# Optimization experiments

Measured on AMD Instinct MI355X. Metric: run time of the kernel, lower is better.

## Reference

```python
import jax, jax.numpy as jnp
import numpy as np

B, F = 512, 512
K, D = 32, 16  # num_kernels, dim_per_kernel


def setup_inputs() -> dict:
    key = jax.random.key(0)
    kx, kt = jax.random.split(key)
    x = jax.random.normal(kx, (B, F), dtype=jnp.float32)
    # keras 'uniform' init is small-range uniform; scale similarly
    T = jax.random.uniform(kt, (F, K * D), dtype=jnp.float32, minval=-0.05, maxval=0.05)
    return {"x": x, "T": T}


def reference(x, T):
    # m: [B, K, D]
    m = (x @ T).reshape(-1, K, D)
    # all-pairs L1 distance per kernel: [B, B, K]
    abs_diffs = jnp.sum(jnp.abs(m[:, None, :, :] - m[None, :, :, :]), axis=-1)
    # minibatch features: sum_j exp(-||m_i - m_j||_1) -> [B, K]
    feats = jnp.sum(jnp.exp(-abs_diffs), axis=1)
    return jnp.concatenate([x, feats], axis=1)
```

## Files before the change

kernel.cpp:

```cpp
#include <hip/hip_runtime.h>
#include <hip/hip_bf16.h>
#include <math.h>

#define BSZ 512
#define FDIM 512
#define NK 32
#define DD 16
#define NDIM (NK*DD)
#define OUTW (FDIM + NK)

typedef __attribute__((ext_vector_type(8))) short short8;
typedef __attribute__((ext_vector_type(4))) float float4v;

static __device__ __forceinline__ short f2bf(float f) {
  return (short)__builtin_bit_cast(unsigned short, __float2bfloat16(f));
}

__global__ __launch_bounds__(256, 4) void k_gemm(
    const float* __restrict__ x, const float* __restrict__ T,
    float* __restrict__ m, float* __restrict__ out) {
  const int t  = threadIdx.x;
  const int b  = blockIdx.x;
  const int rg = b >> 5, cg = b & 31;
  const int r0 = rg * 16, c0 = cg * 16;
  const int lane = t & 63;
  const int w    = __builtin_amdgcn_readfirstlane(t >> 6);
  const int mi   = lane & 15;
  const int q    = lane >> 4;

  const int slice = b >> 3;
  const float4 w0 = ((const float4*)x)[(size_t)slice * 512 + t];
  const float4 w1 = ((const float4*)x)[(size_t)slice * 512 + t + 256];
  const float4 w2 = ((const float4*)T)[(size_t)slice * 512 + t];
  const float4 w3 = ((const float4*)T)[(size_t)slice * 512 + t + 256];
  const float sink = w0.x + w1.y + w2.z + w3.w;

  const float* __restrict__ xa = x + (size_t)(r0 + mi) * FDIM + 128 * w + 8 * q;
  const float* __restrict__ tb = T + (size_t)(128 * w + 8 * q) * NDIM + c0 + mi;
  float4 A[8];
  float  Bv[32];
#pragma unroll
  for (int j = 0; j < 4; ++j) {
    A[2 * j]     = *(const float4*)(xa + 32 * j);
    A[2 * j + 1] = *(const float4*)(xa + 32 * j + 4);
  }
#pragma unroll
  for (int j = 0; j < 4; ++j)
#pragma unroll
    for (int i = 0; i < 8; ++i)
      Bv[8 * j + i] = tb[(size_t)(32 * j + i) * NDIM];

  float4v acc = {0.f, 0.f, 0.f, 0.f};
#pragma unroll
  for (int j = 0; j < 4; ++j) {
    short8 af, bf;
    af[0] = f2bf(A[2*j].x);   af[1] = f2bf(A[2*j].y);
    af[2] = f2bf(A[2*j].z);   af[3] = f2bf(A[2*j].w);
    af[4] = f2bf(A[2*j+1].x); af[5] = f2bf(A[2*j+1].y);
    af[6] = f2bf(A[2*j+1].z); af[7] = f2bf(A[2*j+1].w);
#pragma unroll
    for (int i = 0; i < 8; ++i) bf[i] = f2bf(Bv[8 * j + i]);
    acc = __builtin_amdgcn_mfma_f32_16x16x32_bf16(af, bf, acc, 0, 0, 0);
  }

  __shared__ float red[4][16][16];
#pragma unroll
  for (int r = 0; r < 4; ++r) red[w][q * 4 + r][mi] = acc[r];
  __syncthreads();
  {
    const int orow = t >> 4, ocol = t & 15;
    const float s = red[0][orow][ocol] + red[1][orow][ocol] +
                    red[2][orow][ocol] + red[3][orow][ocol];
    m[(size_t)(r0 + orow) * NDIM + c0 + ocol] = s;
  }

  const int g = b * 256 + t;
  if (g < 65536) {
    const int orow = g >> 7, c4 = g & 127;
    *(float4*)(out + (size_t)orow * OUTW + c4 * 4) =
        *(const float4*)(x + (size_t)orow * FDIM + c4 * 4);
  } else if (g < 65536 + 16384) {
    const int idx = g - 65536;
    const int orow = idx >> 5, kk = idx & 31;
    out[(size_t)orow * OUTW + FDIM + kk] = 0.f;
  }

  asm volatile("" : : "v"(sink));
}

__global__ __launch_bounds__(256) void k_dist(
    const float* __restrict__ m, float* __restrict__ out) {
  __shared__ float Bs[128 * DD];
  __shared__ float red[256];
  const int t   = threadIdx.x;
  const int bid = blockIdx.x;
  const int ig  = bid >> 7;
  const int k   = (bid >> 2) & 31;
  const int jq  = bid & 3;
  const int lane = t & 63;
  const int i    = ig * 64 + lane;

  const float4* ap = (const float4*)(m + (size_t)i * NDIM + k * DD);
  const float4 A0 = ap[0], A1 = ap[1], A2 = ap[2], A3 = ap[3];

  const float* mb = m + (size_t)(jq * 128) * NDIM + k * DD;
#pragma unroll
  for (int qq = 0; qq < 2; ++qq) {
    const int idx = qq * 256 + t;
    const int jrow = idx >> 2, part = idx & 3;
    *(float4*)&Bs[jrow * DD + part * 4] =
        *(const float4*)(mb + (size_t)jrow * NDIM + part * 4);
  }
  __syncthreads();

  float a[DD];
  a[0]=A0.x; a[1]=A0.y; a[2]=A0.z;  a[3]=A0.w;
  a[4]=A1.x; a[5]=A1.y; a[6]=A1.z;  a[7]=A1.w;
  a[8]=A2.x; a[9]=A2.y; a[10]=A2.z; a[11]=A2.w;
  a[12]=A3.x;a[13]=A3.y;a[14]=A3.z; a[15]=A3.w;

  const int w = __builtin_amdgcn_readfirstlane(t >> 6);
  const int jbase = w * 32;
  float f = 0.f;
#pragma unroll 4
  for (int j = 0; j < 32; ++j) {
    const float4* bp = (const float4*)&Bs[(jbase + j) * DD];
    const float4 b0 = bp[0], b1 = bp[1], b2 = bp[2], b3 = bp[3];
    float d =
        fabsf(a[0]  - b0.x) + fabsf(a[1]  - b0.y) +
        fabsf(a[2]  - b0.z) + fabsf(a[3]  - b0.w) +
        fabsf(a[4]  - b1.x) + fabsf(a[5]  - b1.y) +
        fabsf(a[6]  - b1.z) + fabsf(a[7]  - b1.w) +
        fabsf(a[8]  - b2.x) + fabsf(a[9]  - b2.y) +
        fabsf(a[10] - b2.z) + fabsf(a[11] - b2.w) +
        fabsf(a[12] - b3.x) + fabsf(a[13] - b3.y) +
        fabsf(a[14] - b3.z) + fabsf(a[15] - b3.w);
    f += __expf(-d);
  }

  red[t] = f;
  __syncthreads();
  if (t < 64) {
    const float s = red[t] + red[t + 64] + red[t + 128] + red[t + 192];
    atomicAdd(out + (size_t)(ig * 64 + t) * OUTW + FDIM + k, s);
  }
}

extern "C" void kernel_launch(void* const* d_in, const int* in_sizes, int n_in,
                              void* d_out, int out_size, void* d_ws,
                              size_t ws_size, hipStream_t stream) {
  (void)in_sizes; (void)n_in; (void)out_size; (void)ws_size;
  const float* x = (const float*)d_in[0];
  const float* T = (const float*)d_in[1];
  float* out = (float*)d_out;
  float* m   = (float*)d_ws;

  hipLaunchKernelGGL(k_gemm, dim3(1024), dim3(256), 0, stream, x, T, m, out);
  hipLaunchKernelGGL(k_dist, dim3(1024), dim3(256), 0, stream, m, out);
}
```

Measured before the change: 74.82 us.

## Fuse GEMM and pairwise-distance kernels into one persistent kernel with counters

The separate GEMM and distance kernels are merged into one launch of 256 blocks of 1024 threads. Each block computes a 16x64 tile of m, publishes it, and bumps a per-column-group counter. It then spin-waits until its kernel column group is complete, loads all 512 rows of that kernel slice into shared memory, and writes the final feature directly without atomics. This removes a kernel launch boundary, the zero-fill pass and the atomics. In exchange it adds a memset, a cross-block spin wait that depends on all blocks being co-resident, and less parallelism in the distance phase.

Result: slower. 210.5 us (+181.3%).

```diff
diff --git a/kernel.cpp b/kernel.cpp
--- a/kernel.cpp
+++ b/kernel.cpp
@@ -8,6 +8,8 @@
 #define DD 16
 #define NDIM (NK*DD)
 #define OUTW (FDIM + NK)
+#define NBLK 256
+#define NTHR 1024
 
 typedef __attribute__((ext_vector_type(8))) short short8;
 typedef __attribute__((ext_vector_type(4))) float float4v;
@@ -16,115 +18,119 @@
   return (short)__builtin_bit_cast(unsigned short, __float2bfloat16(f));
 }
 
-__global__ __launch_bounds__(256, 4) void k_gemm(
+__global__ __launch_bounds__(1024) void k_fused(
     const float* __restrict__ x, const float* __restrict__ T,
-    float* __restrict__ m, float* __restrict__ out) {
-  const int t  = threadIdx.x;
-  const int b  = blockIdx.x;
-  const int rg = b >> 5, cg = b & 31;
-  const int r0 = rg * 16, c0 = cg * 16;
-  const int lane = t & 63;
-  const int w    = __builtin_amdgcn_readfirstlane(t >> 6);
-  const int mi   = lane & 15;
-  const int q    = lane >> 4;
+    float* __restrict__ m, unsigned* __restrict__ ctr,
+    float* __restrict__ out) {
+  __shared__ float Bs[512 * DD];
+  __shared__ float red2[NTHR];
 
-  const int slice = b >> 3;
-  const float4 w0 = ((const float4*)x)[(size_t)slice * 512 + t];
-  const float4 w1 = ((const float4*)x)[(size_t)slice * 512 + t + 256];
-  const float4 w2 = ((const float4*)T)[(size_t)slice * 512 + t];
-  const float4 w3 = ((const float4*)T)[(size_t)slice * 512 + t + 256];
-  const float sink = w0.x + w1.y + w2.z + w3.w;
+  const int t = threadIdx.x;
+  const int b = blockIdx.x;
 
-  const float* __restrict__ xa = x + (size_t)(r0 + mi) * FDIM + 128 * w + 8 * q;
-  const float* __restrict__ tb = T + (size_t)(128 * w + 8 * q) * NDIM + c0 + mi;
-  float4 A[8];
-  float  Bv[32];
+  {
+    const int g = b * NTHR + t;
+    const float2* xx = (const float2*)x;
+    const float2* tt = (const float2*)T;
+    const float2 v = (g < 131072) ? xx[g] : tt[g - 131072];
+    red2[t] = v.x + v.y;
+  }
+  __syncthreads();
+
+  const int rg = b >> 3, cgg = b & 7;
+  const int r0 = rg * 16, c0 = cgg * 64;
+  const int w  = t >> 6;
+  const int ct = w & 3, kc = w >> 2;
+  const int lane = t & 63, mi = lane & 15, q = lane >> 4;
+
+  {
+    const float* __restrict__ xa =
+        x + (size_t)(r0 + mi) * FDIM + 128 * kc + 8 * q;
+    const float* __restrict__ tb =
+        T + (size_t)(128 * kc + 8 * q) * NDIM + c0 + 16 * ct + mi;
+    float4 A[8];
+    float  Bv[32];
 #pragma unroll
-  for (int j = 0; j < 4; ++j) {
-    A[2 * j]     = *(const float4*)(xa + 32 * j);
-    A[2 * j + 1] = *(const float4*)(xa + 32 * j + 4);
+    for (int j = 0; j < 4; ++j) {
+      A[2 * j]     = *(const float4*)(xa + 32 * j);
+      A[2 * j + 1] = *(const float4*)(xa + 32 * j + 4);
+    }
+#pragma unroll
+    for (int j = 0; j < 4; ++j)
+#pragma unroll
+      for (int i = 0; i < 8; ++i)
+        Bv[8 * j + i] = tb[(size_t)(32 * j + i) * NDIM];
+
+    float4v acc = {0.f, 0.f, 0.f, 0.f};
+#pragma unroll
+    for (int j = 0; j < 4; ++j) {
+      short8 af, bf;
+      af[0] = f2bf(A[2*j].x);   af[1] = f2bf(A[2*j].y);
+      af[2] = f2bf(A[2*j].z);   af[3] = f2bf(A[2*j].w);
+      af[4] = f2bf(A[2*j+1].x); af[5] = f2bf(A[2*j+1].y);
+      af[6] = f2bf(A[2*j+1].z); af[7] = f2bf(A[2*j+1].w);
+#pragma unroll
+      for (int i = 0; i < 8; ++i) bf[i] = f2bf(Bv[8 * j + i]);
+      acc = __builtin_amdgcn_mfma_f32_16x16x32_bf16(af, bf, acc, 0, 0, 0);
+    }
+#pragma unroll
+    for (int r = 0; r < 4; ++r)
+      Bs[(((kc * 4 + ct) * 16) + (q * 4 + r)) * 16 + mi] = acc[r];
   }
-#pragma unroll
-  for (int j = 0; j < 4; ++j)
-#pragma unroll
-    for (int i = 0; i < 8; ++i)
-      Bv[8 * j + i] = tb[(size_t)(32 * j + i) * NDIM];
-
-  float4v acc = {0.f, 0.f, 0.f, 0.f};
-#pragma unroll
-  for (int j = 0; j < 4; ++j) {
-    short8 af, bf;
-    af[0] = f2bf(A[2*j].x);   af[1] = f2bf(A[2*j].y);
-    af[2] = f2bf(A[2*j].z);   af[3] = f2bf(A[2*j].w);
-    af[4] = f2bf(A[2*j+1].x); af[5] = f2bf(A[2*j+1].y);
-    af[6] = f2bf(A[2*j+1].z); af[7] = f2bf(A[2*j+1].w);
-#pragma unroll
-    for (int i = 0; i < 8; ++i) bf[i] = f2bf(Bv[8 * j + i]);
-    acc = __builtin_amdgcn_mfma_f32_16x16x32_bf16(af, bf, acc, 0, 0, 0);
-  }
-
-  __shared__ float red[4][16][16];
-#pragma unroll
-  for (int r = 0; r < 4; ++r) red[w][q * 4 + r][mi] = acc[r];
   __syncthreads();
   {
-    const int orow = t >> 4, ocol = t & 15;
-    const float s = red[0][orow][ocol] + red[1][orow][ocol] +
-                    red[2][orow][ocol] + red[3][orow][ocol];
-    m[(size_t)(r0 + orow) * NDIM + c0 + ocol] = s;
+    const int row = t >> 6, col = t & 63;
+    float s = 0.f;
+#pragma unroll
+    for (int k2 = 0; k2 < 4; ++k2)
+      s += Bs[(((k2 * 4 + (col >> 4)) * 16) + row) * 16 + (col & 15)];
+    m[(size_t)(r0 + row) * NDIM + c0 + col] = s;
   }
-
-  const int g = b * 256 + t;
-  if (g < 65536) {
-    const int orow = g >> 7, c4 = g & 127;
+  if (t < 256) {
+    const int idx = b * 256 + t;
+    const int orow = idx >> 7, c4 = idx & 127;
     *(float4*)(out + (size_t)orow * OUTW + c4 * 4) =
         *(const float4*)(x + (size_t)orow * FDIM + c4 * 4);
-  } else if (g < 65536 + 16384) {
-    const int idx = g - 65536;
-    const int orow = idx >> 5, kk = idx & 31;
-    out[(size_t)orow * OUTW + FDIM + kk] = 0.f;
   }
+  __threadfence();
+  __syncthreads();
+  if (t == 0)
+    __hip_atomic_fetch_add(&ctr[cgg], 1u, __ATOMIC_RELEASE,
+                           __HIP_MEMORY_SCOPE_AGENT);
 
-  asm volatile("" : : "v"(sink));
-}
+  const int ig = b >> 5, kk = b & 31;
+  if (t == 0) {
+    while (__hip_atomic_load(&ctr[kk >> 2], __ATOMIC_ACQUIRE,
+                             __HIP_MEMORY_SCOPE_AGENT) < 32u)
+      __builtin_amdgcn_s_sleep(2);
+  }
+  __syncthreads();
+  __threadfence();
 
-__global__ __launch_bounds__(256) void k_dist(
-    const float* __restrict__ m, float* __restrict__ out) {
-  __shared__ float Bs[128 * DD];
-  __shared__ float red[256];
-  const int t   = threadIdx.x;
-  const int bid = blockIdx.x;
-  const int ig  = bid >> 7;
-  const int k   = (bid >> 2) & 31;
-  const int jq  = bid & 3;
-  const int lane = t & 63;
-  const int i    = ig * 64 + lane;
-
-  const float4* ap = (const float4*)(m + (size_t)i * NDIM + k * DD);
-  const float4 A0 = ap[0], A1 = ap[1], A2 = ap[2], A3 = ap[3];
-
-  const float* mb = m + (size_t)(jq * 128) * NDIM + k * DD;
 #pragma unroll
-  for (int qq = 0; qq < 2; ++qq) {
-    const int idx = qq * 256 + t;
-    const int jrow = idx >> 2, part = idx & 3;
-    *(float4*)&Bs[jrow * DD + part * 4] =
-        *(const float4*)(mb + (size_t)jrow * NDIM + part * 4);
+  for (int it = 0; it < 2; ++it) {
+    const int idx = it * NTHR + t;
+    const int row = idx >> 2, part = idx & 3;
+    *(float4*)&Bs[row * DD + part * 4] =
+        *(const float4*)(m + (size_t)row * NDIM + kk * DD + part * 4);
   }
   __syncthreads();
 
   float a[DD];
-  a[0]=A0.x; a[1]=A0.y; a[2]=A0.z;  a[3]=A0.w;
-  a[4]=A1.x; a[5]=A1.y; a[6]=A1.z;  a[7]=A1.w;
-  a[8]=A2.x; a[9]=A2.y; a[10]=A2.z; a[11]=A2.w;
-  a[12]=A3.x;a[13]=A3.y;a[14]=A3.z; a[15]=A3.w;
+  {
+    const float4* ap = (const float4*)&Bs[(ig * 64 + lane) * DD];
+    const float4 A0 = ap[0], A1 = ap[1], A2 = ap[2], A3 = ap[3];
+    a[0]=A0.x; a[1]=A0.y; a[2]=A0.z;  a[3]=A0.w;
+    a[4]=A1.x; a[5]=A1.y; a[6]=A1.z;  a[7]=A1.w;
+    a[8]=A2.x; a[9]=A2.y; a[10]=A2.z; a[11]=A2.w;
+    a[12]=A3.x;a[13]=A3.y;a[14]=A3.z; a[15]=A3.w;
+  }
 
-  const int w = __builtin_amdgcn_readfirstlane(t >> 6);
-  const int jbase = w * 32;
   float f = 0.f;
+  const int j0 = w * 32;
 #pragma unroll 4
   for (int j = 0; j < 32; ++j) {
-    const float4* bp = (const float4*)&Bs[(jbase + j) * DD];
+    const float4* bp = (const float4*)&Bs[(j0 + j) * DD];
     const float4 b0 = bp[0], b1 = bp[1], b2 = bp[2], b3 = bp[3];
     float d =
         fabsf(a[0]  - b0.x) + fabsf(a[1]  - b0.y) +
@@ -137,12 +143,13 @@
         fabsf(a[14] - b3.z) + fabsf(a[15] - b3.w);
     f += __expf(-d);
   }
-
-  red[t] = f;
+  red2[w * 64 + lane] = f;
   __syncthreads();
   if (t < 64) {
-    const float s = red[t] + red[t + 64] + red[t + 128] + red[t + 192];
-    atomicAdd(out + (size_t)(ig * 64 + t) * OUTW + FDIM + k, s);
+    float s = 0.f;
+#pragma unroll
+    for (int ww = 0; ww < 16; ++ww) s += red2[ww * 64 + t];
+    out[(size_t)(ig * 64 + t) * OUTW + FDIM + kk] = s;
   }
 }
 
@@ -154,7 +161,9 @@
   const float* T = (const float*)d_in[1];
   float* out = (float*)d_out;
   float* m   = (float*)d_ws;
+  unsigned* ctr = (unsigned*)((char*)d_ws + (size_t)BSZ * NDIM * 4);
 
-  hipLaunchKernelGGL(k_gemm, dim3(1024), dim3(256), 0, stream, x, T, m, out);
-  hipLaunchKernelGGL(k_dist, dim3(1024), dim3(256), 0, stream, m, out);
+  hipMemsetAsync(ctr, 0, 8 * sizeof(unsigned), stream);
+  hipLaunchKernelGGL(k_fused, dim3(NBLK), dim3(NTHR), 0, stream,
+                     x, T, m, ctr, out);
 }
```
